# Kernel optimization log

Measured on AMD Instinct MI355X. Metric: run time of the kernel, lower is better.

The kernel has to match this reference:

```python
import jax, jax.numpy as jnp
import numpy as np

NH = 256   # nh_rnn
V = 21     # joints
TC = 60    # cont time dim
CC = 4     # cont channels
DCT_N = 60
T_HIS = 30
HORIZON = 60
BS = 256


def _lin(x, w, b):
    # torch nn.Linear convention: w is [out, in]
    return x @ w.T + b


def setup_inputs() -> dict:
    key = jax.random.key(0)
    ks = iter(jax.random.split(key, 48))

    def rn(shape, s=1.0):
        return jax.random.normal(next(ks), shape, dtype=jnp.float32) * jnp.float32(s)

    inp = {}
    inp["x"] = rn((T_HIS, BS, 63))
    inp["cont"] = rn((BS, TC, V * CC))
    inp["cont_mask"] = jnp.ones((BS, TC), jnp.float32)  # never used (per docstring)
    inp["dct_m"] = rn((DCT_N, T_HIS + HORIZON), 0.1)
    inp["idct_m"] = rn((T_HIS + HORIZON, DCT_N), 0.1)
    inp["root_idx"] = jnp.array([42, 43, 44], dtype=jnp.int32)
    inp["horizon"] = HORIZON

    # --- STSGCN_layer(cont): learned temporal/spatial adjacencies + 1x1 convs + BN(folded) + PReLU ---
    inp["T_c"] = rn((V, TC, TC), 1.0 / np.sqrt(TC))
    inp["A_c"] = rn((TC, V, V), 1.0 / np.sqrt(V))
    inp["conv_w"] = rn((NH, CC), 0.5)
    inp["conv_b"] = rn((NH,), 0.1)
    inp["bn1_scale"] = 1.0 + rn((NH,), 0.1)
    inp["bn1_shift"] = rn((NH,), 0.1)
    inp["resconv_w"] = rn((NH, CC), 0.5)
    inp["resconv_b"] = rn((NH,), 0.1)
    inp["bnr_scale"] = 1.0 + rn((NH,), 0.1)
    inp["bnr_shift"] = rn((NH,), 0.1)
    inp["prelu_a"] = jnp.float32(0.25)

    # tiny MLP encoders
    inp["te1_w"] = rn((10, TC), 1.0 / np.sqrt(TC)); inp["te1_b"] = rn((10,), 0.1)
    inp["te2_w"] = rn((1, 10), 1.0 / np.sqrt(10)); inp["te2_b"] = rn((1,), 0.1)
    inp["ne1_w"] = rn((10, V), 1.0 / np.sqrt(V)); inp["ne1_b"] = rn((10,), 0.1)
    inp["ne2_w"] = rn((1, 10), 1.0 / np.sqrt(10)); inp["ne2_b"] = rn((1,), 0.1)

    # residual MLP head
    din = DCT_N * 3 + NH
    inp["g1_w"] = rn((NH, din), 1.0 / np.sqrt(din)); inp["g1_b"] = rn((NH,), 0.1)
    inp["g2a_w"] = rn((NH, NH), 1.0 / np.sqrt(NH)); inp["g2a_b"] = rn((NH,), 0.1)
    inp["g2b_w"] = rn((NH, NH), 1.0 / np.sqrt(NH)); inp["g2b_b"] = rn((NH,), 0.1)
    inp["g3a_w"] = rn((NH, NH), 1.0 / np.sqrt(NH)); inp["g3a_b"] = rn((NH,), 0.1)
    inp["g3b_w"] = rn((NH, NH), 1.0 / np.sqrt(NH)); inp["g3b_b"] = rn((NH,), 0.1)
    inp["g4_w"] = rn((DCT_N * 3, NH), 1.0 / np.sqrt(NH)); inp["g4_b"] = rn((DCT_N * 3,), 0.1)
    return inp


def reference(x, cont, cont_mask, dct_m, idct_m, root_idx, horizon,
              T_c, A_c, conv_w, conv_b, bn1_scale, bn1_shift,
              resconv_w, resconv_b, bnr_scale, bnr_shift, prelu_a,
              te1_w, te1_b, te2_w, te2_b, ne1_w, ne1_b, ne2_w, ne2_b,
              g1_w, g1_b, g2a_w, g2a_b, g2b_w, g2b_b,
              g3a_w, g3a_b, g3b_w, g3b_b, g4_w, g4_b):
    t_his, bs, _ = x.shape

    # --- root history padded with last frame, then batched DCT ---
    pad_idx = jnp.concatenate([jnp.arange(t_his), jnp.full((horizon,), t_his - 1)])
    root_his = x[:, :, root_idx][pad_idx].transpose(1, 0, 2)                 # [bs, 90, 3]
    root_his_dct = jnp.einsum('dt,btk->bdk', dct_m, root_his).reshape(bs, -1)  # [bs, 180]

    # --- STSGCN layer on contact stream: [b, 4, 60, 21] ---
    xc = cont.reshape(bs, TC, V, CC).transpose(0, 3, 1, 2)                   # [b,c,t,v]
    res = jnp.einsum('nctv,oc->notv', xc, resconv_w) + resconv_b[None, :, None, None]
    res = res * bnr_scale[None, :, None, None] + bnr_shift[None, :, None, None]
    g = jnp.einsum('nctv,vtq->ncqv', xc, T_c)    # temporal adjacency
    g = jnp.einsum('nctv,tvw->nctw', g, A_c)     # spatial adjacency
    h = jnp.einsum('nctv,oc->notv', g, conv_w) + conv_b[None, :, None, None]
    h = h * bn1_scale[None, :, None, None] + bn1_shift[None, :, None, None]
    h = h + res
    h = jnp.where(h >= 0, h, prelu_a * h)        # PReLU, [b, 256, 60, 21]

    # --- time encoder: collapse t=60 -> 1 ---
    ht = h.transpose(0, 1, 3, 2).reshape(bs, NH * V, TC)
    ht = jnp.tanh(_lin(jnp.tanh(_lin(ht, te1_w, te1_b)), te2_w, te2_b))[..., 0]
    # --- node encoder: collapse v=21 -> 1 ---
    hn = ht.reshape(bs, NH, V)
    hcont = jnp.tanh(_lin(jnp.tanh(_lin(hn, ne1_w, ne1_b)), ne2_w, ne2_b))[..., 0]  # [bs, 256]

    # --- residual MLP head on DCT coefficients ---
    rh = jnp.tanh(_lin(jnp.concatenate([root_his_dct, hcont], axis=1), g1_w, g1_b))
    rh = jnp.tanh(_lin(jnp.tanh(_lin(rh, g2a_w, g2a_b)), g2b_w, g2b_b)) + rh
    rh = jnp.tanh(_lin(jnp.tanh(_lin(rh, g3a_w, g3a_b)), g3b_w, g3b_b)) + rh
    root_pred = _lin(rh, g4_w, g4_b) + root_his_dct                          # [bs, 180]
    root_traj = jnp.einsum('td,bdk->btk', idct_m, root_pred.reshape(bs, DCT_N, 3))
    return root_traj                                                          # [bs, 90, 3]
```

## Files before the change

### kernel.cpp

```cpp
#include <hip/hip_runtime.h>

#define NHID 256
#define NV   21
#define NT   60
#define NC   4
#define NDCT 60
#define THIS 30
#define NBS  256

typedef float f32x2 __attribute__((ext_vector_type(2)));
typedef float f32x4 __attribute__((ext_vector_type(4)));

__device__ __forceinline__ float ftanh(float x) {
    float e = __expf(2.0f * x);
    return 1.0f - __fdividef(2.0f, e + 1.0f);
}

__global__ __launch_bounds__(1024, 4) void k_all(
    const float* __restrict__ x,
    const float* __restrict__ cont,
    const float* __restrict__ dct_m, const float* __restrict__ idct_m,
    const int* __restrict__ root_idx,
    const float* __restrict__ T_c, const float* __restrict__ A_c,
    const float* __restrict__ conv_w, const float* __restrict__ conv_b,
    const float* __restrict__ bn1_scale, const float* __restrict__ bn1_shift,
    const float* __restrict__ resconv_w, const float* __restrict__ resconv_b,
    const float* __restrict__ bnr_scale, const float* __restrict__ bnr_shift,
    const float* __restrict__ prelu_a_p,
    const float* __restrict__ te1_w, const float* __restrict__ te1_b,
    const float* __restrict__ te2_w, const float* __restrict__ te2_b,
    const float* __restrict__ ne1_w, const float* __restrict__ ne1_b,
    const float* __restrict__ ne2_w, const float* __restrict__ ne2_b,
    const float* __restrict__ g1_w, const float* __restrict__ g1_b,
    const float* __restrict__ g2a_w, const float* __restrict__ g2a_b,
    const float* __restrict__ g2b_w, const float* __restrict__ g2b_b,
    const float* __restrict__ g3a_w, const float* __restrict__ g3a_b,
    const float* __restrict__ g3b_w, const float* __restrict__ g3b_b,
    const float* __restrict__ g4_w, const float* __restrict__ g4_b,
    float* __restrict__ out)
{
    __shared__ __align__(16) float xc_lds[5040];
    __shared__ __align__(16) float g_lds[5040];
    __shared__ __align__(16) float g2_lds[5040];

    float* in2 = g_lds;
    float* aL  = g_lds + 436;
    float* bL  = g_lds + 692;
    float* rp  = g_lds + 948;

    const int n   = blockIdx.x;
    const int tid = threadIdx.x;

    {
        const float4* src = (const float4*)(cont + n * 5040);
        float4* dst = (float4*)xc_lds;
        for (int i = tid; i < 1260; i += 1024) dst[i] = src[i];
    }
    __syncthreads();

    for (int task = tid; task < 630; task += 1024) {
        int v  = task / 30;
        int q0 = (task - v * 30) * 2;
        const float* tc = T_c + v * 3600 + q0;
        f32x4 a0 = {0.f,0.f,0.f,0.f}, a1 = {0.f,0.f,0.f,0.f};
        #pragma unroll 4
        for (int t = 0; t < 60; ++t) {
            f32x4 xcv = *(const f32x4*)(xc_lds + t * 84 + v * 4);
            float2 tq = *(const float2*)(tc + t * 60);
            a0 += xcv * tq.x;
            a1 += xcv * tq.y;
        }
        *(f32x4*)(g_lds + q0 * 84 + v * 4)       = a0;
        *(f32x4*)(g_lds + (q0 + 1) * 84 + v * 4) = a1;
    }
    __syncthreads();

    for (int task = tid; task < 660; task += 1024) {
        int t  = task / 11;
        int w0 = (task - t * 11) * 2;
        const bool has2 = (w0 < 20);
        const float* ac = A_c + t * 441 + w0;
        f32x4 a0 = {0.f,0.f,0.f,0.f}, a1 = {0.f,0.f,0.f,0.f};
        #pragma unroll
        for (int v = 0; v < 21; ++v) {
            f32x4 gv = *(const f32x4*)(g_lds + t * 84 + v * 4);
            float b0 = ac[v * 21];
            float b1 = has2 ? ac[v * 21 + 1] : 0.f;
            a0 += gv * b0;
            a1 += gv * b1;
        }
        *(f32x4*)(g2_lds + t * 84 + w0 * 4) = a0;
        if (has2) *(f32x4*)(g2_lds + t * 84 + (w0 + 1) * 4) = a1;
    }
    __syncthreads();

    if (tid < 180) {
        int d = tid / 3, k = tid - d * 3;
        int ri = root_idx[k];
        const float* xp = x + n * 63 + ri;
        const float* dm = dct_m + d * 90;
        float acc = 0.f;
        #pragma unroll
        for (int t = 0; t < 30; ++t)
            acc += dm[t] * xp[t * 16128];
        float wl = 0.f;
        #pragma unroll
        for (int t = 30; t < 90; ++t)
            wl += dm[t];
        acc += wl * xp[29 * 16128];
        in2[tid] = acc;
    }

    {
        const int og = tid >> 3;
        const int part = tid & 7;
        const int vstart = (part < 5) ? part * 3 : 15 + (part - 5) * 2;
        const int vcount = (part < 5) ? 3 : 2;

        const float pa = prelu_a_p[0];

        f32x2 cA01[2], cA23[2], cB01[2], cB23[2];
        float cC[2];
        #pragma unroll
        for (int g = 0; g < 2; ++g) {
            int o = og * 2 + g;
            float s1 = bn1_scale[o], sr = bnr_scale[o];
            cA01[g] = (f32x2){conv_w[o*4+0] * s1, conv_w[o*4+1] * s1};
            cA23[g] = (f32x2){conv_w[o*4+2] * s1, conv_w[o*4+3] * s1};
            cB01[g] = (f32x2){resconv_w[o*4+0] * sr, resconv_w[o*4+1] * sr};
            cB23[g] = (f32x2){resconv_w[o*4+2] * sr, resconv_w[o*4+3] * sr};
            cC[g] = conv_b[o] * s1 + bn1_shift[o] + resconv_b[o] * sr + bnr_shift[o];
        }

        float tw2[10], tb1[10];
        #pragma unroll
        for (int j = 0; j < 10; ++j) { tw2[j] = te2_w[j]; tb1[j] = te1_b[j]; }
        const float tb2 = te2_b[0];

        float wacc[2][10];
        #pragma unroll
        for (int g = 0; g < 2; ++g)
            #pragma unroll
            for (int j = 0; j < 10; ++j) wacc[g][j] = 0.f;

        for (int vi = 0; vi < vcount; ++vi) {
            int v = vstart + vi;
            f32x2 u2[2][5];
            #pragma unroll
            for (int g = 0; g < 2; ++g)
                #pragma unroll
                for (int p = 0; p < 5; ++p)
                    u2[g][p] = (f32x2){tb1[2*p], tb1[2*p+1]};

            const float* xcp = xc_lds + v * 4;
            const float* g2p = g2_lds + v * 4;
            for (int t = 0; t < 60; ++t) {
                f32x4 xcv = *(const f32x4*)(xcp + t * 84);
                f32x4 g2v = *(const f32x4*)(g2p + t * 84);
                f32x2 g01 = {g2v.x, g2v.y}, g23 = {g2v.z, g2v.w};
                f32x2 x01 = {xcv.x, xcv.y}, x23 = {xcv.z, xcv.w};
                const float* tewp = te1_w + t;
                f32x2 twp[5];
                #pragma unroll
                for (int p = 0; p < 5; ++p)
                    twp[p] = (f32x2){tewp[p * 120], tewp[p * 120 + 60]};
                #pragma unroll
                for (int g = 0; g < 2; ++g) {
                    f32x2 hv = {cC[g], 0.f};
                    hv += cA01[g] * g01;
                    hv += cA23[g] * g23;
                    hv += cB01[g] * x01;
                    hv += cB23[g] * x23;
                    float h = hv.x + hv.y;
                    h = fmaxf(h, 0.f) + pa * fminf(h, 0.f);
                    #pragma unroll
                    for (int p = 0; p < 5; ++p)
                        u2[g][p] += h * twp[p];
                }
            }

            float nw[10];
            #pragma unroll
            for (int j = 0; j < 10; ++j) nw[j] = ne1_w[j * 21 + v];
            #pragma unroll
            for (int g = 0; g < 2; ++g) {
                float s = tb2;
                #pragma unroll
                for (int p = 0; p < 5; ++p) {
                    s += ftanh(u2[g][p].x) * tw2[2*p];
                    s += ftanh(u2[g][p].y) * tw2[2*p+1];
                }
                s = ftanh(s);
                #pragma unroll
                for (int j = 0; j < 10; ++j) wacc[g][j] += s * nw[j];
            }
        }

        #pragma unroll
        for (int d = 1; d < 8; d <<= 1)
            #pragma unroll
            for (int g = 0; g < 2; ++g)
                #pragma unroll
                for (int j = 0; j < 10; ++j)
                    wacc[g][j] += __shfl_xor(wacc[g][j], d, 64);

        if (part == 0) {
            float nw2[10];
            #pragma unroll
            for (int j = 0; j < 10; ++j) nw2[j] = ne2_w[j];
            float nb2 = ne2_b[0];
            #pragma unroll
            for (int g = 0; g < 2; ++g) {
                int o = og * 2 + g;
                float s = nb2;
                #pragma unroll
                for (int j = 0; j < 10; ++j)
                    s += ftanh(wacc[g][j] + ne1_b[j]) * nw2[j];
                in2[180 + o] = ftanh(s);
            }
        }
    }
    __syncthreads();

    const int gid = tid >> 2;
    const int sub = tid & 3;

#define DENSE(KDIM, NCHUNK, W, SRC, BODY)                                      \
    {                                                                          \
        f32x4 accA = {0.f,0.f,0.f,0.f}, accB = {0.f,0.f,0.f,0.f};              \
        _Pragma("unroll")                                                      \
        for (int s = 0; s < (NCHUNK + 7) / 8; ++s) {                           \
            int c4 = s * 8 + sub;                                              \
            if (c4 < NCHUNK) {                                                 \
                f32x4 av = *(const f32x4*)&SRC[c4 * 4];                        \
                f32x4 wv = *(const f32x4*)&W[gid * KDIM + c4 * 4];             \
                accA += av * wv;                                               \
            }                                                                  \
            int c4b = s * 8 + 4 + sub;                                         \
            if (c4b < NCHUNK) {                                                \
                f32x4 av = *(const f32x4*)&SRC[c4b * 4];                       \
                f32x4 wv = *(const f32x4*)&W[gid * KDIM + c4b * 4];            \
                accB += av * wv;                                               \
            }                                                                  \
        }                                                                      \
        f32x4 accv = accA + accB;                                              \
        float acc = (accv.x + accv.y) + (accv.z + accv.w);                     \
        acc += __shfl_xor(acc, 1, 64);                                         \
        acc += __shfl_xor(acc, 2, 64);                                         \
        if (sub == 0) { int o = gid; float sumv = acc; BODY }                  \
    }                                                                          \
    __syncthreads();

    DENSE(436, 109, g1_w, in2, { aL[o] = ftanh(sumv + g1_b[o]); })
    DENSE(256, 64, g2a_w, aL, { bL[o] = ftanh(sumv + g2a_b[o]); })
    DENSE(256, 64, g2b_w, bL, { aL[o] = ftanh(sumv + g2b_b[o]) + aL[o]; })
    DENSE(256, 64, g3a_w, aL, { bL[o] = ftanh(sumv + g3a_b[o]); })
    DENSE(256, 64, g3b_w, bL, { aL[o] = ftanh(sumv + g3b_b[o]) + aL[o]; })
    DENSE(256, 64, g4_w, aL, { if (o < 180) rp[o] = sumv + g4_b[o] + in2[o]; })

    if (tid < 270) {
        int t = tid / 3;
        int k = tid - t * 3;
        const float* im = idct_m + t * 60;
        const float* rpp = rp + k;
        float acc = 0.f;
        #pragma unroll
        for (int d = 0; d < 60; ++d)
            acc += im[d] * rpp[d * 3];
        out[n * 270 + tid] = acc;
    }
}

extern "C" void kernel_launch(void* const* d_in, const int* in_sizes, int n_in,
                              void* d_out, int out_size, void* d_ws, size_t ws_size,
                              hipStream_t stream)
{
    const float* x        = (const float*)d_in[0];
    const float* cont     = (const float*)d_in[1];
    const float* dct_m    = (const float*)d_in[3];
    const float* idct_m   = (const float*)d_in[4];
    const int*   root_idx = (const int*)d_in[5];
    const float* T_c      = (const float*)d_in[7];
    const float* A_c      = (const float*)d_in[8];
    const float* conv_w   = (const float*)d_in[9];
    const float* conv_b   = (const float*)d_in[10];
    const float* bn1_s    = (const float*)d_in[11];
    const float* bn1_sh   = (const float*)d_in[12];
    const float* rconv_w  = (const float*)d_in[13];
    const float* rconv_b  = (const float*)d_in[14];
    const float* bnr_s    = (const float*)d_in[15];
    const float* bnr_sh   = (const float*)d_in[16];
    const float* prelu_a  = (const float*)d_in[17];
    const float* te1_w    = (const float*)d_in[18];
    const float* te1_b    = (const float*)d_in[19];
    const float* te2_w    = (const float*)d_in[20];
    const float* te2_b    = (const float*)d_in[21];
    const float* ne1_w    = (const float*)d_in[22];
    const float* ne1_b    = (const float*)d_in[23];
    const float* ne2_w    = (const float*)d_in[24];
    const float* ne2_b    = (const float*)d_in[25];
    const float* g1_w     = (const float*)d_in[26];
    const float* g1_b     = (const float*)d_in[27];
    const float* g2a_w    = (const float*)d_in[28];
    const float* g2a_b    = (const float*)d_in[29];
    const float* g2b_w    = (const float*)d_in[30];
    const float* g2b_b    = (const float*)d_in[31];
    const float* g3a_w    = (const float*)d_in[32];
    const float* g3a_b    = (const float*)d_in[33];
    const float* g3b_w    = (const float*)d_in[34];
    const float* g3b_b    = (const float*)d_in[35];
    const float* g4_w     = (const float*)d_in[36];
    const float* g4_b     = (const float*)d_in[37];

    k_all<<<NBS, 1024, 0, stream>>>(x, cont, dct_m, idct_m, root_idx,
                                    T_c, A_c,
                                    conv_w, conv_b, bn1_s, bn1_sh,
                                    rconv_w, rconv_b, bnr_s, bnr_sh,
                                    prelu_a,
                                    te1_w, te1_b, te2_w, te2_b,
                                    ne1_w, ne1_b, ne2_w, ne2_b,
                                    g1_w, g1_b, g2a_w, g2a_b, g2b_w, g2b_b,
                                    g3a_w, g3a_b, g3b_w, g3b_b, g4_w, g4_b,
                                    (float*)d_out);
}
```

Measured before the change: 250.3 us.

## Split fused kernel into conv/encoder and MLP-head kernels; stage te1_w in LDS

Splits the single fused kernel into two launches. The first computes the STSGCN layer, the encoders and the DCT input and writes a per-batch row to a workspace. The second loads that row and runs the residual MLP head and the IDCT. The first kernel also transposes te1_w into shared memory, so the inner t-loop reads it from LDS instead of making strided global loads. The intent is lower register and LDS pressure per kernel and cheaper weight reads, at the cost of an extra launch and a global round trip through the workspace.

```diff
diff --git a/kernel.cpp b/kernel.cpp
--- a/kernel.cpp
+++ b/kernel.cpp
@@ -7,6 +7,7 @@
 #define NDCT 60
 #define THIS 30
 #define NBS  256
+#define WSROW 448
 
 typedef float f32x2 __attribute__((ext_vector_type(2)));
 typedef float f32x4 __attribute__((ext_vector_type(4)));
@@ -16,10 +17,10 @@
     return 1.0f - __fdividef(2.0f, e + 1.0f);
 }
 
-__global__ __launch_bounds__(1024, 4) void k_all(
+__global__ __launch_bounds__(1024, 4) void k_p1(
     const float* __restrict__ x,
     const float* __restrict__ cont,
-    const float* __restrict__ dct_m, const float* __restrict__ idct_m,
+    const float* __restrict__ dct_m,
     const int* __restrict__ root_idx,
     const float* __restrict__ T_c, const float* __restrict__ A_c,
     const float* __restrict__ conv_w, const float* __restrict__ conv_b,
@@ -31,22 +32,11 @@
     const float* __restrict__ te2_w, const float* __restrict__ te2_b,
     const float* __restrict__ ne1_w, const float* __restrict__ ne1_b,
     const float* __restrict__ ne2_w, const float* __restrict__ ne2_b,
-    const float* __restrict__ g1_w, const float* __restrict__ g1_b,
-    const float* __restrict__ g2a_w, const float* __restrict__ g2a_b,
-    const float* __restrict__ g2b_w, const float* __restrict__ g2b_b,
-    const float* __restrict__ g3a_w, const float* __restrict__ g3a_b,
-    const float* __restrict__ g3b_w, const float* __restrict__ g3b_b,
-    const float* __restrict__ g4_w, const float* __restrict__ g4_b,
-    float* __restrict__ out)
+    float* __restrict__ ws)
 {
     __shared__ __align__(16) float xc_lds[5040];
     __shared__ __align__(16) float g_lds[5040];
     __shared__ __align__(16) float g2_lds[5040];
-
-    float* in2 = g_lds;
-    float* aL  = g_lds + 436;
-    float* bL  = g_lds + 692;
-    float* rp  = g_lds + 948;
 
     const int n   = blockIdx.x;
     const int tid = threadIdx.x;
@@ -94,8 +84,14 @@
     }
     __syncthreads();
 
-    if (tid < 180) {
-        int d = tid / 3, k = tid - d * 3;
+    float* tew = g_lds;
+
+    if (tid < 600) {
+        int t = tid / 10, j = tid - t * 10;
+        tew[t * 10 + j] = te1_w[j * 60 + t];
+    } else if (tid >= 600 && tid < 780) {
+        int r = tid - 600;
+        int d = r / 3, k = r - d * 3;
         int ri = root_idx[k];
         const float* xp = x + n * 63 + ri;
         const float* dm = dct_m + d * 90;
@@ -108,8 +104,9 @@
         for (int t = 30; t < 90; ++t)
             wl += dm[t];
         acc += wl * xp[29 * 16128];
-        in2[tid] = acc;
-    }
+        ws[n * WSROW + r] = acc;
+    }
+    __syncthreads();
 
     {
         const int og = tid >> 3;
@@ -157,13 +154,12 @@
             for (int t = 0; t < 60; ++t) {
                 f32x4 xcv = *(const f32x4*)(xcp + t * 84);
                 f32x4 g2v = *(const f32x4*)(g2p + t * 84);
+                f32x2 tw[5];
+                #pragma unroll
+                for (int p = 0; p < 5; ++p)
+                    tw[p] = *(const f32x2*)(tew + t * 10 + p * 2);
                 f32x2 g01 = {g2v.x, g2v.y}, g23 = {g2v.z, g2v.w};
                 f32x2 x01 = {xcv.x, xcv.y}, x23 = {xcv.z, xcv.w};
-                const float* tewp = te1_w + t;
-                f32x2 twp[5];
-                #pragma unroll
-                for (int p = 0; p < 5; ++p)
-                    twp[p] = (f32x2){tewp[p * 120], tewp[p * 120 + 60]};
                 #pragma unroll
                 for (int g = 0; g < 2; ++g) {
                     f32x2 hv = {cC[g], 0.f};
@@ -175,7 +171,7 @@
                     h = fmaxf(h, 0.f) + pa * fminf(h, 0.f);
                     #pragma unroll
                     for (int p = 0; p < 5; ++p)
-                        u2[g][p] += h * twp[p];
+                        u2[g][p] += h * tw[p];
                 }
             }
 
@@ -216,9 +212,32 @@
                 #pragma unroll
                 for (int j = 0; j < 10; ++j)
                     s += ftanh(wacc[g][j] + ne1_b[j]) * nw2[j];
-                in2[180 + o] = ftanh(s);
+                ws[n * WSROW + 180 + o] = ftanh(s);
             }
         }
+    }
+}
+
+__global__ __launch_bounds__(1024, 4) void k_p2(
+    const float* __restrict__ ws,
+    const float* __restrict__ g1_w, const float* __restrict__ g1_b,
+    const float* __restrict__ g2a_w, const float* __restrict__ g2a_b,
+    const float* __restrict__ g2b_w, const float* __restrict__ g2b_b,
+    const float* __restrict__ g3a_w, const float* __restrict__ g3a_b,
+    const float* __restrict__ g3b_w, const float* __restrict__ g3b_b,
+    const float* __restrict__ g4_w, const float* __restrict__ g4_b,
+    const float* __restrict__ idct_m, float* __restrict__ out)
+{
+    __shared__ __align__(16) float in2[436];
+    __shared__ __align__(16) float aL[256];
+    __shared__ __align__(16) float bL[256];
+    __shared__ __align__(16) float rp[180];
+
+    const int n   = blockIdx.x;
+    const int tid = threadIdx.x;
+
+    if (tid < 109) {
+        *(f32x4*)(in2 + tid * 4) = *(const f32x4*)(ws + n * WSROW + tid * 4);
     }
     __syncthreads();
 
@@ -312,14 +331,19 @@
     const float* g4_w     = (const float*)d_in[36];
     const float* g4_b     = (const float*)d_in[37];
 
-    k_all<<<NBS, 1024, 0, stream>>>(x, cont, dct_m, idct_m, root_idx,
-                                    T_c, A_c,
-                                    conv_w, conv_b, bn1_s, bn1_sh,
-                                    rconv_w, rconv_b, bnr_s, bnr_sh,
-                                    prelu_a,
-                                    te1_w, te1_b, te2_w, te2_b,
-                                    ne1_w, ne1_b, ne2_w, ne2_b,
-                                    g1_w, g1_b, g2a_w, g2a_b, g2b_w, g2b_b,
-                                    g3a_w, g3a_b, g3b_w, g3b_b, g4_w, g4_b,
-                                    (float*)d_out);
+    float* wsf = (float*)d_ws;
+
+    k_p1<<<NBS, 1024, 0, stream>>>(x, cont, dct_m, root_idx,
+                                   T_c, A_c,
+                                   conv_w, conv_b, bn1_s, bn1_sh,
+                                   rconv_w, rconv_b, bnr_s, bnr_sh,
+                                   prelu_a,
+                                   te1_w, te1_b, te2_w, te2_b,
+                                   ne1_w, ne1_b, ne2_w, ne2_b,
+                                   wsf);
+
+    k_p2<<<NBS, 1024, 0, stream>>>(wsf,
+                                   g1_w, g1_b, g2a_w, g2a_b, g2b_w, g2b_b,
+                                   g3a_w, g3a_b, g3b_w, g3b_b, g4_w, g4_b,
+                                   idct_m, (float*)d_out);
 }
```

After: 249.5 us. About the same (-0.3%).
